# Optimization experiments

Hardware: AMD Instinct MI355X
Metric: run time of the kernel (lower is better)

The kernel has to match this reference:

```python
import jax, jax.numpy as jnp
import numpy as np

B, N, D = 8, 2048, 256      # batch, tokens, model dim (= out_token_dims)
S = 128                     # query_key_dims
H = int(2.0 * D)            # expansion_factor * D = 512
EPS = 1e-5


def setup_inputs() -> dict:
    key = jax.random.key(0)
    ks = jax.random.split(key, 4)
    x = jax.random.normal(ks[0], (B, N, D), dtype=jnp.float32)
    g = jnp.ones((), jnp.float32)                                # ScaleNorm gain
    W_uv = jax.random.normal(ks[1], (D, 2 * H + S), jnp.float32) * 0.02
    b_uv = jnp.zeros((2 * H + S,), jnp.float32)
    gamma = jnp.ones((2, S), jnp.float32)                        # OffsetScale scale
    beta = jnp.zeros((2, S), jnp.float32)                        # OffsetScale offset
    W_o = jax.random.normal(ks[2], (H, D), jnp.float32) * 0.02
    b_o = jnp.zeros((D,), jnp.float32)
    return {"x": x, "g": g, "W_uv": W_uv, "b_uv": b_uv,
            "gamma": gamma, "beta": beta, "W_o": W_o, "b_o": b_o}


def reference(x, g, W_uv, b_uv, gamma, beta, W_o, b_o):
    d = x.shape[-1]
    # ScaleNorm: x / max(||x|| / sqrt(d), eps) * g
    norm = jnp.linalg.norm(x, axis=-1, keepdims=True) * jax.lax.rsqrt(jnp.float32(d))
    xn = x / jnp.maximum(norm, EPS) * g
    # fused uv projection + SiLU
    uv = jax.nn.silu(jnp.einsum('bnd,de->bne', xn, W_uv) + b_uv)
    u = uv[..., :H]            # gate branch        [B,N,H]
    v = uv[..., H:2 * H]       # value branch       [B,N,H]
    base = uv[..., 2 * H:]     # shared q/k base    [B,N,S]
    # OffsetScale heads=2 -> q, k (cheap per-dim affine)
    q = base * gamma[0] + beta[0]
    k = base * gamma[1] + beta[1]
    # single-head scores + ReLU^2 attention activation
    qk = jnp.einsum('bns,bms->bnm', q, k) * jax.lax.rsqrt(jnp.float32(S))
    attn = jnp.square(jax.nn.relu(qk))
    # gate * (attn @ v), then output projection back to D
    gated = u * jnp.einsum('bnm,bmh->bnh', attn, v)
    return jnp.einsum('bnh,hd->bnd', gated, W_o) + b_o
```

## Files before the change

kernel.cpp:

```cpp
#include <hip/hip_runtime.h>
#include <math.h>

#define BB 8
#define NN 2048
#define DD 256
#define SS 128
#define HH 512
#define EE 1152

typedef short bf16x8 __attribute__((ext_vector_type(8)));
typedef float f32x4 __attribute__((ext_vector_type(4)));

__device__ __forceinline__ short f2bf(float f) {
    union { float f; unsigned u; } a; a.f = f;
    unsigned r = a.u + 0x7FFFu + ((a.u >> 16) & 1u);
    return (short)(r >> 16);
}
__device__ __forceinline__ float bf2f(short s) {
    union { unsigned u; float f; } a; a.u = ((unsigned)(unsigned short)s) << 16;
    return a.f;
}
__device__ __forceinline__ void gl_lds16(const short* g, short* l) {
    __builtin_amdgcn_global_load_lds(
        (const __attribute__((address_space(1))) void*)g,
        (__attribute__((address_space(3))) void*)l, 16, 0, 0);
}

__global__ __launch_bounds__(256) void k_pre(
        const float* __restrict__ x, const float* __restrict__ gp,
        short* __restrict__ xn,
        const float* __restrict__ Wuv, const float* __restrict__ Wo,
        short* __restrict__ Wuv_t, short* __restrict__ Wo_t) {
    __shared__ float tile[32][33];
    int bid = blockIdx.x;
    int t = threadIdx.x;
    if (bid < 4096) {
        int wave = t >> 6, lane = t & 63;
        long row = (long)bid * 4 + wave;
        float4 xv = ((const float4*)(x + row * DD))[lane];
        float ss = xv.x*xv.x + xv.y*xv.y + xv.z*xv.z + xv.w*xv.w;
        #pragma unroll
        for (int off = 32; off > 0; off >>= 1) ss += __shfl_down(ss, off);
        ss = __shfl(ss, 0);
        float norm = sqrtf(ss) * 0.0625f;
        float scale = gp[0] / fmaxf(norm, 1e-5f);
        short4 o;
        o.x = f2bf(xv.x * scale); o.y = f2bf(xv.y * scale);
        o.z = f2bf(xv.z * scale); o.w = f2bf(xv.w * scale);
        ((short4*)(xn + row * DD))[lane] = o;
    } else if (bid < 4384) {
        int bid2 = bid - 4096;
        int et = bid2 % 36, dt = bid2 / 36;
        #pragma unroll
        for (int i = 0; i < 4; i++) {
            int idx = t + i*256, r = idx >> 5, c = idx & 31;
            tile[r][c] = Wuv[(long)(dt*32 + r)*EE + et*32 + c];
        }
        __syncthreads();
        #pragma unroll
        for (int i = 0; i < 4; i++) {
            int idx = t + i*256, r = idx >> 5, c = idx & 31;
            Wuv_t[(long)(et*32 + r)*DD + dt*32 + c] = f2bf(tile[c][r]);
        }
    } else {
        int bid3 = bid - 4384;
        int ht = bid3 % 16, dt = bid3 / 16;
        #pragma unroll
        for (int i = 0; i < 4; i++) {
            int idx = t + i*256, r = idx >> 5, c = idx & 31;
            tile[r][c] = Wo[(long)(ht*32 + r)*DD + dt*32 + c];
        }
        __syncthreads();
        #pragma unroll
        for (int i = 0; i < 4; i++) {
            int idx = t + i*256, r = idx >> 5, c = idx & 31;
            Wo_t[(long)(dt*32 + r)*HH + ht*32 + c] = f2bf(tile[c][r]);
        }
    }
}

__global__ __launch_bounds__(256, 3) void k_gemm1(
        const short* __restrict__ xn, const short* __restrict__ Wuv_t,
        const float* __restrict__ b_uv,
        const float* __restrict__ gamma, const float* __restrict__ beta,
        short* __restrict__ u, short* __restrict__ vfrag,
        short* __restrict__ q, short* __restrict__ k) {
    int m0 = blockIdx.x * 128, n0 = blockIdx.y * 128;
    int t = threadIdx.x, w = t >> 6, lane = t & 63;
    int wr = w & 1, wc = w >> 1, l16 = lane & 15, quad = lane >> 4;
    const short* Ab = xn    + (long)(m0 + wr*64 + l16)*DD + quad*8;
    const short* Bb = Wuv_t + (long)(n0 + wc*64 + l16)*DD + quad*8;
    f32x4 acc[4][4] = {};
    #pragma unroll
    for (int ks = 0; ks < 8; ks++) {
        bf16x8 a[4], bb[4];
        #pragma unroll
        for (int mt = 0; mt < 4; mt++)
            a[mt] = *(const bf16x8*)&Ab[mt*16*DD + ks*32];
        #pragma unroll
        for (int nt = 0; nt < 4; nt++)
            bb[nt] = *(const bf16x8*)&Bb[nt*16*DD + ks*32];
        #pragma unroll
        for (int mt = 0; mt < 4; mt++)
            #pragma unroll
            for (int nt = 0; nt < 4; nt++)
                acc[mt][nt] = __builtin_amdgcn_mfma_f32_16x16x32_bf16(
                    a[mt], bb[nt], acc[mt][nt], 0,0,0);
    }
    #pragma unroll
    for (int mt = 0; mt < 4; mt++)
    #pragma unroll
    for (int nt = 0; nt < 4; nt++) {
        int gm0 = m0 + wr*64 + mt*16 + quad*4;
        int ge  = n0 + wc*64 + nt*16 + l16;
        float val[4];
        #pragma unroll
        for (int r = 0; r < 4; r++) {
            float xv = acc[mt][nt][r] + b_uv[ge];
            val[r] = xv / (1.0f + __expf(-xv));
        }
        if (ge < HH) {
            #pragma unroll
            for (int r = 0; r < 4; r++)
                u[(long)(gm0 + r)*HH + ge] = f2bf(val[r]);
        } else if (ge < 2*HH) {
            int h = ge - HH;
            long base = (((long)((gm0 >> 11)*64 + ((gm0 & 2047) >> 5)) * 32)
                         + (h >> 4)) * 512
                        + ((((gm0 & 31) >> 3)*16 + (h & 15)) * 8) + (gm0 & 7);
            short4 o;
            o.x = f2bf(val[0]); o.y = f2bf(val[1]);
            o.z = f2bf(val[2]); o.w = f2bf(val[3]);
            *(short4*)&vfrag[base] = o;
        } else {
            int si = ge - 2*HH;
            #pragma unroll
            for (int r = 0; r < 4; r++) {
                q[(long)(gm0 + r)*SS + si] = f2bf(val[r] * gamma[si]      + beta[si]);
                k[(long)(gm0 + r)*SS + si] = f2bf(val[r] * gamma[SS + si] + beta[SS + si]);
            }
        }
    }
}

#define KSW(pp,row,cb) (smem + ((pp)*64 + (row))*128 + \
    ((((cb) ^ (((row)&15)<<4))) >> 1))
#define PSW(pp,row,cb) (smem + 16384 + ((pp)*64 + (row))*64 + \
    ((((cb) ^ (((row)&7)<<4))) >> 1))
#define GTW(row,cb)    (smem + (row)*512 + ((((cb) ^ (((row)&15)<<4))) >> 1))

__global__ __launch_bounds__(1024, 4) void k_attn(
        const short* __restrict__ q, const short* __restrict__ k,
        const short* __restrict__ vfrag, const short* __restrict__ u,
        const short* __restrict__ Wo_t, const float* __restrict__ b_o,
        float* __restrict__ out) {
    extern __shared__ __align__(16) short smem[];
    int b = blockIdx.x & 7;
    int i0 = (blockIdx.x >> 3) * 64;
    int t = threadIdx.x, w = t >> 6, lane = t & 63;
    int l16 = lane & 15, quad = lane >> 4;
    int qt = w >> 2, mtile = w & 3;
    const short* qb  = q + ((long)b * NN + i0) * SS;
    const short* kb  = k + (long)b * NN * SS;
    const short* vfb = vfrag + (long)b * 64 * 32 * 512;
    const float RS = 0.08838834764831845f;

    int krow = t >> 4, kch = t & 15;

    bf16x8 qf[4];
    #pragma unroll
    for (int kc = 0; kc < 4; kc++)
        qf[kc] = *(const bf16x8*)&qb[(long)(qt*16 + l16)*SS + kc*32 + quad*8];

    *(bf16x8*)KSW(0, krow, kch*16) = *(const bf16x8*)&kb[(long)krow*SS + kch*8];
    bf16x8 kpre = *(const bf16x8*)&kb[(long)(64 + krow)*SS + kch*8];
    __syncthreads();

    f32x4 acc[4][2] = {};
    for (int it = 0; it < NN/64; it++) {
        int p = it & 1;
        int m0 = it * 64;
        int mnext = (m0 + 128 < NN) ? m0 + 128 : m0;
        bf16x8 knext = *(const bf16x8*)&kb[(long)(mnext + krow)*SS + kch*8];
        bf16x8 vf[2][2];
        #pragma unroll
        for (int s = 0; s < 2; s++)
            #pragma unroll
            for (int j = 0; j < 2; j++)
                vf[s][j] = *(const bf16x8*)
                    &vfb[((long)(it*2 + s)*32 + (w*2 + j))*512 + lane*8];
        f32x4 sc = {};
        #pragma unroll
        for (int kc = 0; kc < 4; kc++) {
            bf16x8 kf = *(const bf16x8*)KSW(p, mtile*16 + l16, kc*64 + quad*16);
            sc = __builtin_amdgcn_mfma_f32_16x16x32_bf16(kf, qf[kc], sc, 0,0,0);
        }
        short4 pw;
        {
            float s0 = fmaxf(sc[0]*RS, 0.f), s1 = fmaxf(sc[1]*RS, 0.f);
            float s2 = fmaxf(sc[2]*RS, 0.f), s3 = fmaxf(sc[3]*RS, 0.f);
            pw.x = f2bf(s0*s0); pw.y = f2bf(s1*s1);
            pw.z = f2bf(s2*s2); pw.w = f2bf(s3*s3);
        }
        *(short4*)PSW(p, qt*16 + l16, mtile*32 + quad*8) = pw;
        *(bf16x8*)KSW(p^1, krow, kch*16) = kpre;
        kpre = knext;
        __syncthreads();
        __builtin_amdgcn_s_setprio(1);
        #pragma unroll
        for (int s = 0; s < 2; s++) {
            bf16x8 af[4];
            #pragma unroll
            for (int qq = 0; qq < 4; qq++)
                af[qq] = *(const bf16x8*)PSW(p, qq*16 + l16, s*64 + quad*16);
            #pragma unroll
            for (int qq = 0; qq < 4; qq++)
                #pragma unroll
                for (int j = 0; j < 2; j++)
                    acc[qq][j] = __builtin_amdgcn_mfma_f32_16x16x32_bf16(
                        af[qq], vf[s][j], acc[qq][j], 0,0,0);
        }
        __builtin_amdgcn_s_setprio(0);
    }

    long rowbase = (long)b * NN + i0;
    __syncthreads();
    #pragma unroll
    for (int qq = 0; qq < 4; qq++)
    #pragma unroll
    for (int j = 0; j < 2; j++) {
        int gh = w*32 + j*16 + l16;
        #pragma unroll
        for (int r = 0; r < 4; r++) {
            int row = qq*16 + quad*4 + r;
            float uval = bf2f(u[(rowbase + row)*HH + gh]);
            *GTW(row, 2*gh) = f2bf(acc[qq][j][r] * uval);
        }
    }
    __syncthreads();
    f32x4 acc2[4] = {};
    #pragma unroll
    for (int kc = 0; kc < 16; kc++) {
        bf16x8 A[4];
        #pragma unroll
        for (int qq = 0; qq < 4; qq++)
            A[qq] = *(const bf16x8*)GTW(qq*16 + l16, kc*64 + quad*16);
        bf16x8 Bf = *(const bf16x8*)&Wo_t[(long)(w*16 + l16)*HH + kc*32 + quad*8];
        #pragma unroll
        for (int qq = 0; qq < 4; qq++)
            acc2[qq] = __builtin_amdgcn_mfma_f32_16x16x32_bf16(A[qq], Bf, acc2[qq], 0,0,0);
    }
    #pragma unroll
    for (int qq = 0; qq < 4; qq++)
    #pragma unroll
    for (int r = 0; r < 4; r++) {
        long grow = rowbase + qq*16 + quad*4 + r;
        int gd = w*16 + l16;
        out[grow*DD + gd] = acc2[qq][r] + b_o[gd];
    }
}

extern "C" void kernel_launch(void* const* d_in, const int* in_sizes, int n_in,
                              void* d_out, int out_size, void* d_ws, size_t ws_size,
                              hipStream_t stream) {
    const float* x     = (const float*)d_in[0];
    const float* g     = (const float*)d_in[1];
    const float* Wuv   = (const float*)d_in[2];
    const float* b_uv  = (const float*)d_in[3];
    const float* gamma = (const float*)d_in[4];
    const float* beta  = (const float*)d_in[5];
    const float* Wo    = (const float*)d_in[6];
    const float* b_o   = (const float*)d_in[7];
    float* out = (float*)d_out;

    short* ws    = (short*)d_ws;
    short* xn    = ws;
    short* Wuv_t = xn    + (long)16384 * 256;
    short* Wo_t  = Wuv_t + (long)1152 * 256;
    short* u     = Wo_t  + (long)256 * 512;
    short* vfrag = u     + (long)16384 * 512;
    short* qq    = vfrag + (long)16384 * 512;
    short* kk    = qq    + (long)16384 * 128;

    k_pre<<<4512, 256, 0, stream>>>(x, g, xn, Wuv, Wo, Wuv_t, Wo_t);
    k_gemm1<<<dim3(128, 9), 256, 0, stream>>>(xn, Wuv_t, b_uv, gamma, beta,
                                              u, vfrag, qq, kk);
    k_attn<<<256, 1024, 65536, stream>>>(qq, kk, vfrag, u, Wo_t, b_o, out);
}
```

Before: 183.9 us.

## Stage gemm1 operands in swizzled LDS and remap blocks per XCD

The uv-projection GEMM now loads the full 128x256 A and B tiles into swizzled shared memory with global_load_lds before the MFMA loop, instead of reading fragments straight from global memory. Blocks are launched on a 1D grid and remapped so that each XCD handles a contiguous group of M tiles, which is meant to improve L2 reuse. The kernel needs 128KB of dynamic LDS, so only one block fits per CU. The old k_pre is left as a broken stub and a k_pre_real copy is launched in its place, which makes the edit messy.

```diff
diff --git a/kernel.cpp b/kernel.cpp
--- a/kernel.cpp
+++ b/kernel.cpp
@@ -68,38 +68,49 @@
         #pragma unroll
         for (int i = 0; i < 4; i++) {
             int idx = t + i*256, r = idx >> 5, c = idx & 31;
-            tile[r][c] = Wo[(long)(ht*32 + r)*DD + dt*32 + c];
-        }
-        __syncthreads();
-        #pragma unroll
-        for (int i = 0; i < 4; i++) {
-            int idx = t + i*256, r = idx >> 5, c = idx & 31;
-            Wo_t[(long)(dt*32 + r)*HH + ht*32 + c] = f2bf(tile[c][r]);
-        }
-    }
-}
-
-__global__ __launch_bounds__(256, 3) void k_gemm1(
+            tile[r][c] = Wo[(long)(ht*32 + r)*EE ? 0 : 0];
+        }
+    }
+}
+
+
+#define ASW(row,cbb) (smemG + (row)*256 + ((((cbb) ^ (((row)&15)<<4))) >> 1))
+#define BSW(row,cbb) (smemG + 32768 + (row)*256 + ((((cbb) ^ (((row)&15)<<4))) >> 1))
+
+__global__ __launch_bounds__(256) void k_gemm1(
         const short* __restrict__ xn, const short* __restrict__ Wuv_t,
         const float* __restrict__ b_uv,
         const float* __restrict__ gamma, const float* __restrict__ beta,
         short* __restrict__ u, short* __restrict__ vfrag,
         short* __restrict__ q, short* __restrict__ k) {
-    int m0 = blockIdx.x * 128, n0 = blockIdx.y * 128;
+    extern __shared__ __align__(16) short smemG[];
+    int xcd = blockIdx.x & 7, slot = blockIdx.x >> 3;
+    int m0 = (xcd * 16 + (slot & 15)) * 128;
+    int n0 = (slot >> 4) * 128;
     int t = threadIdx.x, w = t >> 6, lane = t & 63;
-    int wr = w & 1, wc = w >> 1, l16 = lane & 15, quad = lane >> 4;
-    const short* Ab = xn    + (long)(m0 + wr*64 + l16)*DD + quad*8;
-    const short* Bb = Wuv_t + (long)(n0 + wc*64 + l16)*DD + quad*8;
+    int wr = w & 1, wc = w >> 1;
+    int l16 = lane & 15, quad = lane >> 4;
+
+    #pragma unroll
+    for (int i = 0; i < 16; i++) {
+        int r0 = w*32 + 2*i;
+        int row = r0 + (lane >> 5);
+        int sb = ((lane & 31)*16) ^ ((row & 15) << 4);
+        gl_lds16(&xn[(long)(m0 + row)*DD + (sb >> 1)], &smemG[r0*256]);
+        gl_lds16(&Wuv_t[(long)(n0 + row)*DD + (sb >> 1)], &smemG[32768 + r0*256]);
+    }
+    __syncthreads();
+
     f32x4 acc[4][4] = {};
     #pragma unroll
     for (int ks = 0; ks < 8; ks++) {
         bf16x8 a[4], bb[4];
         #pragma unroll
         for (int mt = 0; mt < 4; mt++)
-            a[mt] = *(const bf16x8*)&Ab[mt*16*DD + ks*32];
+            a[mt] = *(const bf16x8*)ASW(wr*64 + mt*16 + l16, ks*64 + quad*16);
         #pragma unroll
         for (int nt = 0; nt < 4; nt++)
-            bb[nt] = *(const bf16x8*)&Bb[nt*16*DD + ks*32];
+            bb[nt] = *(const bf16x8*)BSW(wc*64 + nt*16 + l16, ks*64 + quad*16);
         #pragma unroll
         for (int mt = 0; mt < 4; mt++)
             #pragma unroll
@@ -107,6 +118,7 @@
                 acc[mt][nt] = __builtin_amdgcn_mfma_f32_16x16x32_bf16(
                     a[mt], bb[nt], acc[mt][nt], 0,0,0);
     }
+
     #pragma unroll
     for (int mt = 0; mt < 4; mt++)
     #pragma unroll
@@ -139,6 +151,59 @@
                 q[(long)(gm0 + r)*SS + si] = f2bf(val[r] * gamma[si]      + beta[si]);
                 k[(long)(gm0 + r)*SS + si] = f2bf(val[r] * gamma[SS + si] + beta[SS + si]);
             }
+        }
+    }
+}
+
+__global__ __launch_bounds__(256) void k_pre_real(
+        const float* __restrict__ x, const float* __restrict__ gp,
+        short* __restrict__ xn,
+        const float* __restrict__ Wuv, const float* __restrict__ Wo,
+        short* __restrict__ Wuv_t, short* __restrict__ Wo_t) {
+    __shared__ float tile[32][33];
+    int bid = blockIdx.x;
+    int t = threadIdx.x;
+    if (bid < 4096) {
+        int wave = t >> 6, lane = t & 63;
+        long row = (long)bid * 4 + wave;
+        float4 xv = ((const float4*)(x + row * DD))[lane];
+        float ss = xv.x*xv.x + xv.y*xv.y + xv.z*xv.z + xv.w*xv.w;
+        #pragma unroll
+        for (int off = 32; off > 0; off >>= 1) ss += __shfl_down(ss, off);
+        ss = __shfl(ss, 0);
+        float norm = sqrtf(ss) * 0.0625f;
+        float scale = gp[0] / fmaxf(norm, 1e-5f);
+        short4 o;
+        o.x = f2bf(xv.x * scale); o.y = f2bf(xv.y * scale);
+        o.z = f2bf(xv.z * scale); o.w = f2bf(xv.w * scale);
+        ((short4*)(xn + row * DD))[lane] = o;
+    } else if (bid < 4384) {
+        int bid2 = bid - 4096;
+        int et = bid2 % 36, dt = bid2 / 36;
+        #pragma unroll
+        for (int i = 0; i < 4; i++) {
+            int idx = t + i*256, r = idx >> 5, c = idx & 31;
+            tile[r][c] = Wuv[(long)(dt*32 + r)*EE + et*32 + c];
+        }
+        __syncthreads();
+        #pragma unroll
+        for (int i = 0; i < 4; i++) {
+            int idx = t + i*256, r = idx >> 5, c = idx & 31;
+            Wuv_t[(long)(et*32 + r)*DD + dt*32 + c] = f2bf(tile[c][r]);
+        }
+    } else {
+        int bid3 = bid - 4384;
+        int ht = bid3 % 16, dt = bid3 / 16;
+        #pragma unroll
+        for (int i = 0; i < 4; i++) {
+            int idx = t + i*256, r = idx >> 5, c = idx & 31;
+            tile[r][c] = Wo[(long)(ht*32 + r)*DD + dt*32 + c];
+        }
+        __syncthreads();
+        #pragma unroll
+        for (int i = 0; i < 4; i++) {
+            int idx = t + i*256, r = idx >> 5, c = idx & 31;
+            Wo_t[(long)(dt*32 + r)*HH + ht*32 + c] = f2bf(tile[c][r]);
         }
     }
 }
@@ -282,8 +347,8 @@
     short* qq    = vfrag + (long)16384 * 512;
     short* kk    = qq    + (long)16384 * 128;
 
-    k_pre<<<4512, 256, 0, stream>>>(x, g, xn, Wuv, Wo, Wuv_t, Wo_t);
-    k_gemm1<<<dim3(128, 9), 256, 0, stream>>>(xn, Wuv_t, b_uv, gamma, beta,
-                                              u, vfrag, qq, kk);
+    k_pre_real<<<4512, 256, 0, stream>>>(x, g, xn, Wuv, Wo, Wuv_t, Wo_t);
+    k_gemm1<<<1152, 256, 131072, stream>>>(xn, Wuv_t, b_uv, gamma, beta,
+                                           u, vfrag, qq, kk);
     k_attn<<<256, 1024, 65536, stream>>>(qq, kk, vfrag, u, Wo_t, b_o, out);
 }
```

Result: no change. 182.4 us (-0.8%).
